# Kernel optimization log

Hardware: AMD Instinct MI355X
Metric: run time of the kernel (lower is better)

Reference implementation:

```python
import jax, jax.numpy as jnp
import numpy as np

NUM_HEADS = 8
HIDDEN = 384
PROJ = 256
N_TOKENS = 4096  # input_size = H*W*D
EPS_NORM = 1e-12
EPS_LN = 1e-5


def setup_inputs() -> dict:
    key = jax.random.key(0)
    ks = jax.random.split(key, 10)
    B, C, H, W, D = 4, HIDDEN, 16, 16, 16
    std_c = 1.0 / np.sqrt(C)
    std_n = 1.0 / np.sqrt(N_TOKENS)
    std_4c = 1.0 / np.sqrt(4 * C)
    return {
        "x": jax.random.normal(ks[0], (B, C, H, W, D), dtype=jnp.float32),
        "y": jax.random.normal(ks[1], (B, C, H, W, D), dtype=jnp.float32),
        # weights stored [in, out] (transposed vs torch nn.Linear)
        "Wq": jax.random.uniform(ks[2], (C, C), jnp.float32, -std_c, std_c),
        "Wkv": jax.random.uniform(ks[3], (C, 2 * C), jnp.float32, -std_c, std_c),
        "EF": jax.random.uniform(ks[4], (N_TOKENS, PROJ), jnp.float32, -std_n, std_n),
        "temperature": jnp.ones((NUM_HEADS, 1, 1), dtype=jnp.float32),
        "norm_gamma": jnp.ones((C,), dtype=jnp.float32),
        "norm_beta": jnp.zeros((C,), dtype=jnp.float32),
        "mlp_w1": jax.random.uniform(ks[5], (C, 4 * C), jnp.float32, -std_c, std_c),
        "mlp_b1": jnp.zeros((4 * C,), dtype=jnp.float32),
        "mlp_w2": jax.random.uniform(ks[6], (4 * C, C), jnp.float32, -std_4c, std_4c),
        "mlp_b2": jnp.zeros((C,), dtype=jnp.float32),
    }


def _forward(x, y, Wq, Wkv, EF, temperature, norm_gamma, norm_beta,
             mlp_w1, mlp_b1, mlp_w2, mlp_b2):
    B, C, H, W, D = x.shape
    N = H * W * D
    nh = NUM_HEADS
    hd = C // nh

    xt = x.reshape(B, C, N).transpose(0, 2, 1)  # [B,N,C]
    yt = y.reshape(B, C, N).transpose(0, 2, 1)  # [B,N,C]

    q = (xt @ Wq).reshape(B, N, nh, hd).transpose(0, 2, 3, 1)      # [B,h,d,N]
    kv = (xt @ Wkv).reshape(B, N, 2, nh, hd)
    k = kv[:, :, 0].transpose(0, 2, 3, 1)                          # [B,h,d,N]
    v = kv[:, :, 1].transpose(0, 2, 3, 1)                          # [B,h,d,N]

    # Linformer-style EF projection of K/V over the token axis
    kp = jnp.einsum('bhdn,nk->bhdk', k, EF)                        # [B,h,d,P]
    vp = jnp.einsum('bhdn,nk->bhdk', v, EF)                        # [B,h,d,P]

    # L2-normalize Q along the TOKEN axis (faithful to F.normalize(dim=-1) on [B,h,d,N])
    qn = q / jnp.maximum(jnp.linalg.norm(q, axis=-1, keepdims=True), EPS_NORM)

    attn = jnp.einsum('bhdn,bhdk->bhnk', qn, kp) * temperature     # [B,h,N,P]
    attn = jax.nn.softmax(attn, axis=-1)

    o = jnp.einsum('bhnk,bhdk->bhnd', attn, vp)                    # [B,h,N,d]
    # faithful to source: permute(0,3,1,2) then raw reshape to [B,N,C]
    o = o.transpose(0, 3, 1, 2).reshape(B, N, C)

    # LayerNorm
    mu = jnp.mean(o, axis=-1, keepdims=True)
    var = jnp.mean(jnp.square(o - mu), axis=-1, keepdims=True)
    ln = (o - mu) / jnp.sqrt(var + EPS_LN) * norm_gamma + norm_beta

    # MLP (MONAI MLPBlock, eval mode: dropout off), exact GELU
    h1 = jax.nn.gelu(ln @ mlp_w1 + mlp_b1, approximate=False)
    mlp_out = h1 @ mlp_w2 + mlp_b2

    yt = yt + mlp_out
    return yt.reshape(B, H, W, D, C).transpose(0, 4, 1, 2, 3)      # [B,C,H,W,D]


def reference(x, y, Wq, Wkv, EF, temperature, norm_gamma, norm_beta,
              mlp_w1, mlp_b1, mlp_w2, mlp_b2):
    return _forward(x, y, Wq, Wkv, EF, temperature, norm_gamma, norm_beta,
                    mlp_w1, mlp_b1, mlp_w2, mlp_b2)
```

## Files before the change

kernel.cpp:

```cpp
#include <hip/hip_runtime.h>

#define NH 8
#define CDIM 384
#define HDIM 48
#define NTOK 4096
#define PDIM 256
#define BDIM 4

typedef unsigned short u16;
typedef unsigned int u32;
typedef __bf16 bf16x8 __attribute__((ext_vector_type(8)));
typedef float f32x4 __attribute__((ext_vector_type(4)));

__device__ __forceinline__ u16 f2b(float f) {
    u32 u = __float_as_uint(f);
    u = (u + 0x7fffu + ((u >> 16) & 1u)) >> 16;
    return (u16)u;
}

__device__ __forceinline__ bf16x8 bzero8() {
    bf16x8 v;
#pragma unroll
    for (int i = 0; i < 8; i++) v[i] = (__bf16)0.0f;
    return v;
}

__device__ __forceinline__ void gload16(const u16* g, u16* l) {
    __builtin_amdgcn_global_load_lds(
        (const __attribute__((address_space(1))) void*)g,
        (__attribute__((address_space(3))) void*)l, 16, 0, 0);
}

__global__ __launch_bounds__(256) void transpose_cast(
    const float* __restrict__ in, u16* __restrict__ outT, u16* __restrict__ outC,
    int R, int Cc)
{
    __shared__ float tile[32][33];
    int r0 = blockIdx.y * 32, c0 = blockIdx.x * 32;
    size_t zoff = (size_t)blockIdx.z * R * Cc;
    const float* inp = in + zoff;
    int tx = threadIdx.x, ty = threadIdx.y;
#pragma unroll
    for (int i = 0; i < 4; i++) {
        int r = r0 + ty + i * 8;
        float v = inp[(size_t)r * Cc + c0 + tx];
        tile[ty + i * 8][tx] = v;
        if (outC) outC[zoff + (size_t)r * Cc + c0 + tx] = f2b(v);
    }
    __syncthreads();
    u16* oT = outT + zoff;
#pragma unroll
    for (int i = 0; i < 4; i++) {
        int c = c0 + ty + i * 8;
        oT[(size_t)c * R + r0 + tx] = f2b(tile[tx][ty + i * 8]);
    }
}

template <int EPI>
__global__ __launch_bounds__(256) void gemm_bt(
    const u16* __restrict__ A, const u16* __restrict__ Bt,
    int M, int Nn, int K, long sA, long sB, long sC,
    float* __restrict__ Cf, const float* __restrict__ bias,
    u16* __restrict__ Cbf, const float* __restrict__ Yin, float* __restrict__ Out)
{
    const int BM = 128, BK = 32, LP = 32;
    __shared__ u16 lsA[128 * LP];
    __shared__ u16 lsB[128 * LP];
    const int tid = threadIdx.x;
    const int wave = tid >> 6, lane = tid & 63;
    const int lm = lane & 15, lkb = lane >> 4;
    const int bm = blockIdx.x, bn = blockIdx.y, bz = blockIdx.z;
    int bb = bz, ks = 0, ke = K;
    if (EPI == 4) { bb = bz >> 4; ks = (bz & 15) * (K >> 4); ke = ks + (K >> 4); }
    const u16* Ab = A + (size_t)bb * sA;
    const u16* Bb = Bt + (size_t)bb * sB;
    const int wm = (wave >> 1) * 64, wn = (wave & 1) * 64;

    f32x4 acc[4][4];
#pragma unroll
    for (int i = 0; i < 4; i++)
#pragma unroll
        for (int j = 0; j < 4; j++) acc[i][j] = f32x4{0.f, 0.f, 0.f, 0.f};

    for (int k0 = ks; k0 < ke; k0 += BK) {
#pragma unroll
        for (int j = 0; j < 2; j++) {
            int cb = (j * 4 + wave) * 64;
            int q = cb + lane;
            int r = q >> 2, ch = q & 3;
            gload16(Ab + (size_t)(bm * BM + r) * K + k0 + ch * 8, &lsA[cb * 8]);
            gload16(Bb + (size_t)(bn * BM + r) * K + k0 + ch * 8, &lsB[cb * 8]);
        }
        __syncthreads();
        bf16x8 af[4], bfr[4];
#pragma unroll
        for (int t = 0; t < 4; t++) {
            af[t]  = *(const bf16x8*)&lsA[(wm + t * 16 + lm) * LP + lkb * 8];
            bfr[t] = *(const bf16x8*)&lsB[(wn + t * 16 + lm) * LP + lkb * 8];
        }
#pragma unroll
        for (int mi = 0; mi < 4; mi++)
#pragma unroll
            for (int ni = 0; ni < 4; ni++)
                acc[mi][ni] = __builtin_amdgcn_mfma_f32_16x16x32_bf16(
                    af[mi], bfr[ni], acc[mi][ni], 0, 0, 0);
        __syncthreads();
    }

#pragma unroll
    for (int mi = 0; mi < 4; mi++)
#pragma unroll
        for (int ni = 0; ni < 4; ni++)
#pragma unroll
            for (int r = 0; r < 4; r++) {
                int m = bm * BM + wm + mi * 16 + lkb * 4 + r;
                int n = bn * BM + wn + ni * 16 + lm;
                float v = acc[mi][ni][r];
                if (EPI == 0) {
                    Cf[(size_t)bz * sC + (size_t)m * Nn + n] = v;
                } else if (EPI == 1) {
                    float x = v + bias[n];
                    float g = 0.5f * x * (1.0f + erff(x * 0.70710678118654752f));
                    Cbf[(size_t)m * Nn + n] = f2b(g);
                } else if (EPI == 2) {
                    int b = m >> 12, tok = m & 4095;
                    size_t oi = ((size_t)b * CDIM + n) * NTOK + tok;
                    Out[oi] = v + bias[n] + Yin[oi];
                } else if (EPI == 3) {
                    size_t oi = (size_t)bz * sC + (size_t)m * Nn + n;
                    Cf[oi] = v;
                    Cbf[oi] = f2b(v);
                } else {
                    Cf[(size_t)bz * sC + (size_t)m * Nn + n] = v;
                }
            }
}

__global__ __launch_bounds__(256) void gred(
    const float* __restrict__ part, u16* __restrict__ Gtb)
{
    int idx = blockIdx.x * 256 + threadIdx.x;
    int b = idx / (PDIM * CDIM);
    int e = idx % (PDIM * CDIM);
    float s = 0.f;
#pragma unroll
    for (int j = 0; j < 16; j++)
        s += part[((size_t)(b * 16 + j)) * (PDIM * CDIM) + e];
    Gtb[idx] = f2b(s);
}

__global__ __launch_bounds__(128) void colsumsq(
    const float* __restrict__ q, float* __restrict__ pcs)
{
    int c = blockIdx.x * 128 + threadIdx.x;
    int b = blockIdx.z;
    int chunk = blockIdx.y;
    const float* qp = q + ((size_t)b * NTOK + chunk * 256) * CDIM + c;
    float s = 0.f;
#pragma unroll 4
    for (int i = 0; i < 256; i++) { float v = qp[(size_t)i * CDIM]; s += v * v; }
    pcs[(size_t)chunk * (BDIM * CDIM) + b * CDIM + c] = s;
}

__global__ __launch_bounds__(256) void colsumred(
    const float* __restrict__ pcs, float* __restrict__ css)
{
    int idx = blockIdx.x * 256 + threadIdx.x;
    if (idx < BDIM * CDIM) {
        float s = 0.f;
#pragma unroll
        for (int j = 0; j < 16; j++) s += pcs[(size_t)j * (BDIM * CDIM) + idx];
        css[idx] = s;
    }
}

__global__ __launch_bounds__(256) void scalepack2(
    const float* __restrict__ kpvp, const float* __restrict__ css,
    const float* __restrict__ temp, u16* __restrict__ kps, u16* __restrict__ vpb)
{
    int idx = blockIdx.x * 256 + threadIdx.x;
    int c = idx % CDIM;
    int t = idx / CDIM;
    int p = t & 255;
    int b = t >> 8;
    int h = c / HDIM, d = c % HDIM;
    const float* row = kpvp + ((size_t)b * PDIM + p) * (2 * CDIM);
    float kv = row[c];
    float vv = row[CDIM + c];
    float nrm = fmaxf(sqrtf(css[b * CDIM + c]), 1e-12f);
    float sc = temp[h] / nrm;
    int bh = b * NH + h;
    kps[((size_t)bh * PDIM + p) * HDIM + d] = f2b(kv * sc);
    vpb[((size_t)bh * HDIM + d) * PDIM + p] = f2b(vv);
}

__global__ __launch_bounds__(256) void attn_fused(
    const u16* __restrict__ qbf, const u16* __restrict__ kps,
    const u16* __restrict__ vpb, float* __restrict__ o_scr)
{
    __shared__ u16 vp_l[48 * 264];
    __shared__ u16 un[64 * 264];
    u16* kp_l = un;
    u16* p_l = un;

    int nt = blockIdx.x, h = blockIdx.y, b = blockIdx.z;
    int tid = threadIdx.x, wave = tid >> 6, lane = tid & 63;
    int lm = lane & 15, lkb = lane >> 4;
    const u16* kpsb = kps + (size_t)(b * NH + h) * PDIM * HDIM;
    const u16* vpbb = vpb + (size_t)(b * NH + h) * HDIM * PDIM;

    for (int i = tid; i < 1536; i += 256) {
        int row = i / 6, ch = i % 6;
        *(uint4*)&kp_l[row * 56 + ch * 8] = *(const uint4*)(kpsb + row * 48 + ch * 8);
    }
    for (int i = tid; i < 1536; i += 256) {
        int row = i / 32, ch = i % 32;
        *(uint4*)&vp_l[row * 264 + ch * 8] = *(const uint4*)(vpbb + row * 256 + ch * 8);
    }
    __syncthreads();

    int t0 = nt * 64 + wave * 16;
    const u16* qb = qbf + ((size_t)b * NTOK + t0 + lm) * CDIM + h * HDIM;
    bf16x8 a0 = *(const bf16x8*)(qb + lkb * 8);
    bf16x8 a1 = bzero8();
    if (lkb < 2) a1 = *(const bf16x8*)(qb + 32 + lkb * 8);

    f32x4 s[16];
#pragma unroll
    for (int pi = 0; pi < 16; pi++) {
        f32x4 acc = f32x4{0.f, 0.f, 0.f, 0.f};
        bf16x8 b0 = *(const bf16x8*)&kp_l[(pi * 16 + lm) * 56 + lkb * 8];
        acc = __builtin_amdgcn_mfma_f32_16x16x32_bf16(a0, b0, acc, 0, 0, 0);
        bf16x8 b1 = bzero8();
        if (lkb < 2) b1 = *(const bf16x8*)&kp_l[(pi * 16 + lm) * 56 + 32 + lkb * 8];
        acc = __builtin_amdgcn_mfma_f32_16x16x32_bf16(a1, b1, acc, 0, 0, 0);
        s[pi] = acc;
    }
    __syncthreads();

#pragma unroll
    for (int r = 0; r < 4; r++) {
        float mx = s[0][r];
#pragma unroll
        for (int pi = 1; pi < 16; pi++) mx = fmaxf(mx, s[pi][r]);
        for (int m = 1; m < 16; m <<= 1) mx = fmaxf(mx, __shfl_xor(mx, m, 64));
        float e[16];
        float sum = 0.f;
#pragma unroll
        for (int pi = 0; pi < 16; pi++) { e[pi] = __expf(s[pi][r] - mx); sum += e[pi]; }
        for (int m = 1; m < 16; m <<= 1) sum += __shfl_xor(sum, m, 64);
        float inv = 1.0f / sum;
        int tl = wave * 16 + lkb * 4 + r;
#pragma unroll
        for (int pi = 0; pi < 16; pi++)
            p_l[tl * 264 + pi * 16 + lm] = f2b(e[pi] * inv);
    }
    __syncthreads();

    f32x4 oa[3];
#pragma unroll
    for (int di = 0; di < 3; di++) oa[di] = f32x4{0.f, 0.f, 0.f, 0.f};
#pragma unroll
    for (int ksl = 0; ksl < 8; ksl++) {
        bf16x8 pa = *(const bf16x8*)&p_l[(wave * 16 + lm) * 264 + ksl * 32 + lkb * 8];
#pragma unroll
        for (int di = 0; di < 3; di++) {
            bf16x8 vb = *(const bf16x8*)&vp_l[(di * 16 + lm) * 264 + ksl * 32 + lkb * 8];
            oa[di] = __builtin_amdgcn_mfma_f32_16x16x32_bf16(pa, vb, oa[di], 0, 0, 0);
        }
    }
    size_t obase = (size_t)b * ((size_t)NTOK * CDIM);
#pragma unroll
    for (int di = 0; di < 3; di++)
#pragma unroll
        for (int r = 0; r < 4; r++) {
            int n = t0 + lkb * 4 + r;
            int d = di * 16 + lm;
            o_scr[obase + ((size_t)(d * NH + h)) * NTOK + n] = oa[di][r];
        }
}

__global__ __launch_bounds__(128) void ln_kernel(
    const float* __restrict__ o, const float* __restrict__ gamma,
    const float* __restrict__ beta, u16* __restrict__ outbf)
{
    int row = blockIdx.x;
    const float* rp = o + (size_t)row * CDIM;
    int tid = threadIdx.x;
    float v0 = rp[tid], v1 = rp[tid + 128], v2 = rp[tid + 256];
    float s = v0 + v1 + v2;
    for (int m = 1; m < 64; m <<= 1) s += __shfl_xor(s, m, 64);
    __shared__ float red[2];
    if ((tid & 63) == 0) red[tid >> 6] = s;
    __syncthreads();
    float mean = (red[0] + red[1]) * (1.0f / CDIM);
    float d0 = v0 - mean, d1 = v1 - mean, d2 = v2 - mean;
    float qv = d0 * d0 + d1 * d1 + d2 * d2;
    for (int m = 1; m < 64; m <<= 1) qv += __shfl_xor(qv, m, 64);
    __shared__ float red2[2];
    if ((tid & 63) == 0) red2[tid >> 6] = qv;
    __syncthreads();
    float var = (red2[0] + red2[1]) * (1.0f / CDIM);
    float rstd = rsqrtf(var + 1e-5f);
    u16* op = outbf + (size_t)row * CDIM;
    op[tid]       = f2b(d0 * rstd * gamma[tid]       + beta[tid]);
    op[tid + 128] = f2b(d1 * rstd * gamma[tid + 128] + beta[tid + 128]);
    op[tid + 256] = f2b(d2 * rstd * gamma[tid + 256] + beta[tid + 256]);
}

extern "C" void kernel_launch(void* const* d_in, const int* in_sizes, int n_in,
                              void* d_out, int out_size, void* d_ws, size_t ws_size,
                              hipStream_t stream)
{
    (void)in_sizes; (void)n_in; (void)out_size; (void)ws_size;
    const float* x    = (const float*)d_in[0];
    const float* y    = (const float*)d_in[1];
    const float* Wq   = (const float*)d_in[2];
    const float* Wkv  = (const float*)d_in[3];
    const float* EF   = (const float*)d_in[4];
    const float* temp = (const float*)d_in[5];
    const float* gam  = (const float*)d_in[6];
    const float* bet  = (const float*)d_in[7];
    const float* w1   = (const float*)d_in[8];
    const float* b1   = (const float*)d_in[9];
    const float* w2   = (const float*)d_in[10];
    const float* b2   = (const float*)d_in[11];
    float* out = (float*)d_out;

    char* w = (char*)d_ws;
    size_t off = 0;
    auto alloc = [&](size_t nb) { size_t o = off; off += (nb + 255) & ~(size_t)255; return o; };
    u16*   xt_bf = (u16*)(w + alloc((size_t)BDIM * NTOK * CDIM * 2));
    u16*   x_bf  = (u16*)(w + alloc((size_t)BDIM * NTOK * CDIM * 2));
    u16*   Wqt   = (u16*)(w + alloc((size_t)CDIM * CDIM * 2));
    u16*   EFt   = (u16*)(w + alloc((size_t)PDIM * NTOK * 2));
    u16*   w1t   = (u16*)(w + alloc((size_t)1536 * CDIM * 2));
    u16*   w2t   = (u16*)(w + alloc((size_t)CDIM * 1536 * 2));
    u16*   Wkvt  = (u16*)(w + alloc((size_t)768 * CDIM * 2));
    float* qf    = (float*)(w + alloc((size_t)BDIM * NTOK * CDIM * 4));
    float* gpart = (float*)(w + alloc((size_t)BDIM * NTOK * 1536 * 2));
    u16*   h1bf  = (u16*)gpart;
    u16*   Gt_bf = (u16*)(w + alloc((size_t)BDIM * PDIM * CDIM * 2));
    float* kpvpf = (float*)(w + alloc((size_t)BDIM * PDIM * 2 * CDIM * 4));
    float* pcs   = (float*)(w + alloc((size_t)16 * BDIM * CDIM * 4));
    float* css   = (float*)(w + alloc((size_t)BDIM * CDIM * 4));
    u16*   kps   = (u16*)(w + alloc((size_t)BDIM * NH * PDIM * HDIM * 2));
    u16*   vpb   = (u16*)(w + alloc((size_t)BDIM * NH * HDIM * PDIM * 2));
    u16*   q_bf  = xt_bf;
    float* o_scr = qf;
    u16*   ln_bf = x_bf;

    dim3 tb(32, 8, 1);
    transpose_cast<<<dim3(NTOK / 32, CDIM / 32, BDIM), tb, 0, stream>>>(x, xt_bf, x_bf, CDIM, NTOK);
    transpose_cast<<<dim3(CDIM / 32, CDIM / 32, 1), tb, 0, stream>>>(Wq, Wqt, nullptr, CDIM, CDIM);
    transpose_cast<<<dim3(PDIM / 32, NTOK / 32, 1), tb, 0, stream>>>(EF, EFt, nullptr, NTOK, PDIM);
    transpose_cast<<<dim3(1536 / 32, CDIM / 32, 1), tb, 0, stream>>>(w1, w1t, nullptr, CDIM, 1536);
    transpose_cast<<<dim3(CDIM / 32, 1536 / 32, 1), tb, 0, stream>>>(w2, w2t, nullptr, 1536, CDIM);
    transpose_cast<<<dim3(768 / 32, CDIM / 32, 1), tb, 0, stream>>>(Wkv, Wkvt, nullptr, CDIM, 768);

    gemm_bt<4><<<dim3(PDIM / 128, CDIM / 128, BDIM * 16), 256, 0, stream>>>(
        EFt, x_bf, PDIM, CDIM, NTOK, 0, (long)CDIM * NTOK, (long)PDIM * CDIM,
        gpart, nullptr, nullptr, nullptr, nullptr);
    gred<<<dim3((BDIM * PDIM * CDIM) / 256, 1, 1), 256, 0, stream>>>(gpart, Gt_bf);

    gemm_bt<3><<<dim3(NTOK / 128, CDIM / 128, BDIM), 256, 0, stream>>>(
        xt_bf, Wqt, NTOK, CDIM, CDIM, (long)NTOK * CDIM, 0, (long)NTOK * CDIM,
        qf, nullptr, q_bf, nullptr, nullptr);

    colsumsq<<<dim3(CDIM / 128, 16, BDIM), 128, 0, stream>>>(qf, pcs);
    colsumred<<<dim3(6, 1, 1), 256, 0, stream>>>(pcs, css);

    gemm_bt<0><<<dim3(PDIM / 128, 768 / 128, BDIM), 256, 0, stream>>>(
        Gt_bf, Wkvt, PDIM, 768, CDIM, (long)PDIM * CDIM, 0, (long)PDIM * 768,
        kpvpf, nullptr, nullptr, nullptr, nullptr);

    scalepack2<<<dim3((BDIM * PDIM * CDIM) / 256, 1, 1), 256, 0, stream>>>(
        kpvpf, css, temp, kps, vpb);

    attn_fused<<<dim3(NTOK / 64, NH, BDIM), 256, 0, stream>>>(q_bf, kps, vpb, o_scr);

    ln_kernel<<<dim3(BDIM * NTOK, 1, 1), 128, 0, stream>>>(o_scr, gam, bet, ln_bf);

    gemm_bt<1><<<dim3((BDIM * NTOK) / 128, 1536 / 128, 1), 256, 0, stream>>>(
        ln_bf, w1t, BDIM * NTOK, 1536, CDIM, 0, 0, 0,
        nullptr, b1, h1bf, nullptr, nullptr);
    gemm_bt<2><<<dim3((BDIM * NTOK) / 128, CDIM / 128, 1), 256, 0, stream>>>(
        h1bf, w2t, BDIM * NTOK, CDIM, 1536, 0, 0, 0,
        nullptr, b2, nullptr, y, out);
}
```

Baseline: 236.7 us.

## Double-buffer GEMM loads, add half-M tiles, tanh GELU, vectorized epilogues, bf16 Q

```diff
diff --git a/kernel.cpp b/kernel.cpp
--- a/kernel.cpp
+++ b/kernel.cpp
@@ -12,11 +12,16 @@
 typedef __bf16 bf16x8 __attribute__((ext_vector_type(8)));
 typedef float f32x4 __attribute__((ext_vector_type(4)));
 
+#define VMFENCE asm volatile("s_waitcnt vmcnt(0)" ::: "memory")
+
 __device__ __forceinline__ u16 f2b(float f) {
     u32 u = __float_as_uint(f);
     u = (u + 0x7fffu + ((u >> 16) & 1u)) >> 16;
     return (u16)u;
 }
+__device__ __forceinline__ float b2f(u16 u) {
+    return __uint_as_float(((u32)u) << 16);
+}
 
 __device__ __forceinline__ bf16x8 bzero8() {
     bf16x8 v;
@@ -29,6 +34,13 @@
     __builtin_amdgcn_global_load_lds(
         (const __attribute__((address_space(1))) void*)g,
         (__attribute__((address_space(3))) void*)l, 16, 0, 0);
+}
+
+__device__ __forceinline__ float gelu_f(float x) {
+    float z = 0.7978845608028654f * (x + 0.044715f * x * x * x);
+    float e = __expf(2.0f * z);
+    float t = 1.0f - 2.0f / (e + 1.0f);
+    return 0.5f * x * (1.0f + t);
 }
 
 __global__ __launch_bounds__(256) void transpose_cast(
@@ -56,16 +68,18 @@
     }
 }
 
-template <int EPI>
+template <int EPI, int HALFM>
 __global__ __launch_bounds__(256) void gemm_bt(
     const u16* __restrict__ A, const u16* __restrict__ Bt,
     int M, int Nn, int K, long sA, long sB, long sC,
     float* __restrict__ Cf, const float* __restrict__ bias,
     u16* __restrict__ Cbf, const float* __restrict__ Yin, float* __restrict__ Out)
 {
-    const int BM = 128, BK = 32, LP = 32;
-    __shared__ u16 lsA[128 * LP];
-    __shared__ u16 lsB[128 * LP];
+    const int BMv = HALFM ? 64 : 128;
+    const int MT  = HALFM ? 2 : 4;
+    const int BK = 32, LP = 32;
+    __shared__ u16 lsA[2][BMv * LP];
+    __shared__ u16 lsB[2][128 * LP];
     const int tid = threadIdx.x;
     const int wave = tid >> 6, lane = tid & 63;
     const int lm = lane & 15, lkb = lane >> 4;
@@ -74,66 +88,103 @@
     if (EPI == 4) { bb = bz >> 4; ks = (bz & 15) * (K >> 4); ke = ks + (K >> 4); }
     const u16* Ab = A + (size_t)bb * sA;
     const u16* Bb = Bt + (size_t)bb * sB;
-    const int wm = (wave >> 1) * 64, wn = (wave & 1) * 64;
-
-    f32x4 acc[4][4];
-#pragma unroll
-    for (int i = 0; i < 4; i++)
+    const int wm = (wave >> 1) * (HALFM ? 32 : 64), wn = (wave & 1) * 64;
+
+    f32x4 acc[MT][4];
+#pragma unroll
+    for (int i = 0; i < MT; i++)
 #pragma unroll
         for (int j = 0; j < 4; j++) acc[i][j] = f32x4{0.f, 0.f, 0.f, 0.f};
 
-    for (int k0 = ks; k0 < ke; k0 += BK) {
+    auto stage = [&](int k0, int c) {
+        if (HALFM) {
+            int cb = wave * 64;
+            int q = cb + lane;
+            int r = q >> 2, ch = q & 3;
+            gload16(Ab + (size_t)(bm * BMv + r) * K + k0 + ch * 8, &lsA[c][cb * 8]);
+        } else {
+#pragma unroll
+            for (int j = 0; j < 2; j++) {
+                int cb = (j * 4 + wave) * 64;
+                int q = cb + lane;
+                int r = q >> 2, ch = q & 3;
+                gload16(Ab + (size_t)(bm * BMv + r) * K + k0 + ch * 8, &lsA[c][cb * 8]);
+            }
+        }
 #pragma unroll
         for (int j = 0; j < 2; j++) {
             int cb = (j * 4 + wave) * 64;
             int q = cb + lane;
             int r = q >> 2, ch = q & 3;
-            gload16(Ab + (size_t)(bm * BM + r) * K + k0 + ch * 8, &lsA[cb * 8]);
-            gload16(Bb + (size_t)(bn * BM + r) * K + k0 + ch * 8, &lsB[cb * 8]);
+            gload16(Bb + (size_t)(bn * 128 + r) * K + k0 + ch * 8, &lsB[c][cb * 8]);
         }
-        __syncthreads();
-        bf16x8 af[4], bfr[4];
-#pragma unroll
-        for (int t = 0; t < 4; t++) {
-            af[t]  = *(const bf16x8*)&lsA[(wm + t * 16 + lm) * LP + lkb * 8];
-            bfr[t] = *(const bf16x8*)&lsB[(wn + t * 16 + lm) * LP + lkb * 8];
-        }
-#pragma unroll
-        for (int mi = 0; mi < 4; mi++)
+    };
+
+    const int nt = (ke - ks) / BK;
+    int cur = 0;
+    stage(ks, 0);
+    VMFENCE;
+    __syncthreads();
+
+    for (int t = 0; t < nt; ++t) {
+        if (t + 1 < nt) stage(ks + (t + 1) * BK, cur ^ 1);
+        bf16x8 af[MT], bfr[4];
+#pragma unroll
+        for (int m = 0; m < MT; m++)
+            af[m] = *(const bf16x8*)&lsA[cur][(wm + m * 16 + lm) * LP + lkb * 8];
+#pragma unroll
+        for (int n = 0; n < 4; n++)
+            bfr[n] = *(const bf16x8*)&lsB[cur][(wn + n * 16 + lm) * LP + lkb * 8];
+#pragma unroll
+        for (int mi = 0; mi < MT; mi++)
 #pragma unroll
             for (int ni = 0; ni < 4; ni++)
                 acc[mi][ni] = __builtin_amdgcn_mfma_f32_16x16x32_bf16(
                     af[mi], bfr[ni], acc[mi][ni], 0, 0, 0);
+        VMFENCE;
         __syncthreads();
-    }
-
-#pragma unroll
-    for (int mi = 0; mi < 4; mi++)
-#pragma unroll
-        for (int ni = 0; ni < 4; ni++)
-#pragma unroll
-            for (int r = 0; r < 4; r++) {
-                int m = bm * BM + wm + mi * 16 + lkb * 4 + r;
-                int n = bn * BM + wn + ni * 16 + lm;
-                float v = acc[mi][ni][r];
-                if (EPI == 0) {
-                    Cf[(size_t)bz * sC + (size_t)m * Nn + n] = v;
-                } else if (EPI == 1) {
-                    float x = v + bias[n];
-                    float g = 0.5f * x * (1.0f + erff(x * 0.70710678118654752f));
-                    Cbf[(size_t)m * Nn + n] = f2b(g);
-                } else if (EPI == 2) {
-                    int b = m >> 12, tok = m & 4095;
-                    size_t oi = ((size_t)b * CDIM + n) * NTOK + tok;
-                    Out[oi] = v + bias[n] + Yin[oi];
-                } else if (EPI == 3) {
-                    size_t oi = (size_t)bz * sC + (size_t)m * Nn + n;
-                    Cf[oi] = v;
-                    Cbf[oi] = f2b(v);
-                } else {
-                    Cf[(size_t)bz * sC + (size_t)m * Nn + n] = v;
+        cur ^= 1;
+    }
+
+    if (EPI == 2) {
+#pragma unroll
+        for (int mi = 0; mi < MT; mi++)
+#pragma unroll
+            for (int ni = 0; ni < 4; ni++) {
+                int m0 = bm * BMv + wm + mi * 16 + lkb * 4;
+                int n = bn * 128 + wn + ni * 16 + lm;
+                int b = m0 >> 12, tok = m0 & 4095;
+                size_t oi = ((size_t)b * CDIM + n) * NTOK + tok;
+                float4 yv = *(const float4*)(Yin + oi);
+                float bv = bias[n];
+                float4 ov;
+                ov.x = acc[mi][ni][0] + bv + yv.x;
+                ov.y = acc[mi][ni][1] + bv + yv.y;
+                ov.z = acc[mi][ni][2] + bv + yv.z;
+                ov.w = acc[mi][ni][3] + bv + yv.w;
+                *(float4*)(Out + oi) = ov;
+            }
+    } else {
+#pragma unroll
+        for (int mi = 0; mi < MT; mi++)
+#pragma unroll
+            for (int ni = 0; ni < 4; ni++)
+#pragma unroll
+                for (int r = 0; r < 4; r++) {
+                    int m = bm * BMv + wm + mi * 16 + lkb * 4 + r;
+                    int n = bn * 128 + wn + ni * 16 + lm;
+                    float v = acc[mi][ni][r];
+                    if (EPI == 0) {
+                        Cf[(size_t)bz * sC + (size_t)m * Nn + n] = v;
+                    } else if (EPI == 1) {
+                        Cbf[(size_t)m * Nn + n] = f2b(gelu_f(v + bias[n]));
+                    } else if (EPI == 4) {
+                        Cf[(size_t)bz * sC + (size_t)m * Nn + n] = v;
+                    } else {
+                        Cbf[(size_t)bz * sC + (size_t)m * Nn + n] = f2b(v);
+                    }
                 }
-            }
+    }
 }
 
 __global__ __launch_bounds__(256) void gred(
@@ -150,15 +201,15 @@
 }
 
 __global__ __launch_bounds__(128) void colsumsq(
-    const float* __restrict__ q, float* __restrict__ pcs)
+    const u16* __restrict__ q, float* __restrict__ pcs)
 {
     int c = blockIdx.x * 128 + threadIdx.x;
     int b = blockIdx.z;
     int chunk = blockIdx.y;
-    const float* qp = q + ((size_t)b * NTOK + chunk * 256) * CDIM + c;
+    const u16* qp = q + ((size_t)b * NTOK + chunk * 256) * CDIM + c;
     float s = 0.f;
 #pragma unroll 4
-    for (int i = 0; i < 256; i++) { float v = qp[(size_t)i * CDIM]; s += v * v; }
+    for (int i = 0; i < 256; i++) { float v = b2f(qp[(size_t)i * CDIM]); s += v * v; }
     pcs[(size_t)chunk * (BDIM * CDIM) + b * CDIM + c] = s;
 }
 
@@ -271,13 +322,13 @@
     }
     size_t obase = (size_t)b * ((size_t)NTOK * CDIM);
 #pragma unroll
-    for (int di = 0; di < 3; di++)
-#pragma unroll
-        for (int r = 0; r < 4; r++) {
-            int n = t0 + lkb * 4 + r;
-            int d = di * 16 + lm;
-            o_scr[obase + ((size_t)(d * NH + h)) * NTOK + n] = oa[di][r];
-        }
+    for (int di = 0; di < 3; di++) {
+        int d = di * 16 + lm;
+        int n0 = t0 + lkb * 4;
+        float4 ov;
+        ov.x = oa[di][0]; ov.y = oa[di][1]; ov.z = oa[di][2]; ov.w = oa[di][3];
+        *(float4*)(o_scr + obase + (size_t)(d * NH + h) * NTOK + n0) = ov;
+    }
 }
 
 __global__ __launch_bounds__(128) void ln_kernel(
@@ -332,12 +383,12 @@
     auto alloc = [&](size_t nb) { size_t o = off; off += (nb + 255) & ~(size_t)255; return o; };
     u16*   xt_bf = (u16*)(w + alloc((size_t)BDIM * NTOK * CDIM * 2));
     u16*   x_bf  = (u16*)(w + alloc((size_t)BDIM * NTOK * CDIM * 2));
+    u16*   q_bf  = (u16*)(w + alloc((size_t)BDIM * NTOK * CDIM * 2));
     u16*   Wqt   = (u16*)(w + alloc((size_t)CDIM * CDIM * 2));
     u16*   EFt   = (u16*)(w + alloc((size_t)PDIM * NTOK * 2));
     u16*   w1t   = (u16*)(w + alloc((size_t)1536 * CDIM * 2));
     u16*   w2t   = (u16*)(w + alloc((size_t)CDIM * 1536 * 2));
     u16*   Wkvt  = (u16*)(w + alloc((size_t)768 * CDIM * 2));
-    float* qf    = (float*)(w + alloc((size_t)BDIM * NTOK * CDIM * 4));
     float* gpart = (float*)(w + alloc((size_t)BDIM * NTOK * 1536 * 2));
     u16*   h1bf  = (u16*)gpart;
     u16*   Gt_bf = (u16*)(w + alloc((size_t)BDIM * PDIM * CDIM * 2));
@@ -346,8 +397,7 @@
     float* css   = (float*)(w + alloc((size_t)BDIM * CDIM * 4));
     u16*   kps   = (u16*)(w + alloc((size_t)BDIM * NH * PDIM * HDIM * 2));
     u16*   vpb   = (u16*)(w + alloc((size_t)BDIM * NH * HDIM * PDIM * 2));
-    u16*   q_bf  = xt_bf;
-    float* o_scr = qf;
+    float* o_scr = (float*)(w + alloc((size_t)BDIM * NTOK * CDIM * 4));
     u16*   ln_bf = x_bf;
 
     dim3 tb(32, 8, 1);
@@ -358,19 +408,19 @@
     transpose_cast<<<dim3(CDIM / 32, 1536 / 32, 1), tb, 0, stream>>>(w2, w2t, nullptr, 1536, CDIM);
     transpose_cast<<<dim3(768 / 32, CDIM / 32, 1), tb, 0, stream>>>(Wkv, Wkvt, nullptr, CDIM, 768);
 
-    gemm_bt<4><<<dim3(PDIM / 128, CDIM / 128, BDIM * 16), 256, 0, stream>>>(
+    gemm_bt<4, 1><<<dim3(PDIM / 64, CDIM / 128, BDIM * 16), 256, 0, stream>>>(
         EFt, x_bf, PDIM, CDIM, NTOK, 0, (long)CDIM * NTOK, (long)PDIM * CDIM,
         gpart, nullptr, nullptr, nullptr, nullptr);
     gred<<<dim3((BDIM * PDIM * CDIM) / 256, 1, 1), 256, 0, stream>>>(gpart, Gt_bf);
 
-    gemm_bt<3><<<dim3(NTOK / 128, CDIM / 128, BDIM), 256, 0, stream>>>(
+    gemm_bt<5, 1><<<dim3(NTOK / 64, CDIM / 128, BDIM), 256, 0, stream>>>(
         xt_bf, Wqt, NTOK, CDIM, CDIM, (long)NTOK * CDIM, 0, (long)NTOK * CDIM,
-        qf, nullptr, q_bf, nullptr, nullptr);
-
-    colsumsq<<<dim3(CDIM / 128, 16, BDIM), 128, 0, stream>>>(qf, pcs);
+        nullptr, nullptr, q_bf, nullptr, nullptr);
+
+    colsumsq<<<dim3(CDIM / 128, 16, BDIM), 128, 0, stream>>>(q_bf, pcs);
     colsumred<<<dim3(6, 1, 1), 256, 0, stream>>>(pcs, css);
 
-    gemm_bt<0><<<dim3(PDIM / 128, 768 / 128, BDIM), 256, 0, stream>>>(
+    gemm_bt<0, 1><<<dim3(PDIM / 64, 768 / 128, BDIM), 256, 0, stream>>>(
         Gt_bf, Wkvt, PDIM, 768, CDIM, (long)PDIM * CDIM, 0, (long)PDIM * 768,
         kpvpf, nullptr, nullptr, nullptr, nullptr);
 
@@ -381,10 +431,10 @@
 
     ln_kernel<<<dim3(BDIM * NTOK, 1, 1), 128, 0, stream>>>(o_scr, gam, bet, ln_bf);
 
-    gemm_bt<1><<<dim3((BDIM * NTOK) / 128, 1536 / 128, 1), 256, 0, stream>>>(
+    gemm_bt<1, 0><<<dim3((BDIM * NTOK) / 128, 1536 / 128, 1), 256, 0, stream>>>(
         ln_bf, w1t, BDIM * NTOK, 1536, CDIM, 0, 0, 0,
         nullptr, b1, h1bf, nullptr, nullptr);
-    gemm_bt<2><<<dim3((BDIM * NTOK) / 128, CDIM / 128, 1), 256, 0, stream>>>(
+    gemm_bt<2, 1><<<dim3((BDIM * NTOK) / 64, CDIM / 128, 1), 256, 0, stream>>>(
         h1bf, w2t, BDIM * NTOK, CDIM, 1536, 0, 0, 0,
         nullptr, b2, nullptr, y, out);
 }
```

Measured after the change: 220.4 us. 6.9% less time.
